# Kernel optimization log

Hardware: AMD Instinct MI355X
Metric: run time of the kernel (lower is better)

Reference implementation:

```python
import jax, jax.numpy as jnp
import numpy as np

CHANNELS = 256
C_QK = CHANNELS // 8


def setup_inputs() -> dict:
    key = jax.random.key(0)
    ks = jax.random.split(key, 7)
    b, c, h, w = 8, CHANNELS, 64, 64
    x = jax.random.normal(ks[0], (b, c, h, w), dtype=jnp.float32)
    # 1x1 conv weights stored as [out_ch, in_ch]; biases [out_ch]
    s = 1.0 / np.sqrt(c)
    wq = jax.random.uniform(ks[1], (C_QK, c), jnp.float32, -s, s)
    bq = jax.random.uniform(ks[2], (C_QK,), jnp.float32, -s, s)
    wk = jax.random.uniform(ks[3], (C_QK, c), jnp.float32, -s, s)
    bk = jax.random.uniform(ks[4], (C_QK,), jnp.float32, -s, s)
    wv = jax.random.uniform(ks[5], (c, c), jnp.float32, -s, s)
    bv = jax.random.uniform(ks[6], (c,), jnp.float32, -s, s)
    return {"x": x, "wq": wq, "bq": bq, "wk": wk, "bk": bk, "wv": wv, "bv": bv}


def reference(x, wq, bq, wk, bk, wv, bv):
    b, c, h, w = x.shape
    xf = x.reshape(b, c, h * w)  # [b, c, n]
    # 1x1 convs == per-pixel linear projections
    q = jnp.einsum('oc,bcn->bon', wq, xf) + bq[None, :, None]  # [b, c//8, n]
    k = jnp.einsum('oc,bcn->bon', wk, xf) + bk[None, :, None]  # [b, c//8, n]
    v = jnp.einsum('oc,bcn->bon', wv, xf) + bv[None, :, None]  # [b, c, n]
    # attention[i, j] = q_i . k_j  (no scaling, matching the torch code)
    attn = jnp.einsum('bdi,bdj->bij', q, k)  # [b, n, n]
    attn = jax.nn.softmax(attn, axis=-1)
    # out[:, :, i] = sum_j attn[i, j] * v[:, :, j]
    out = jnp.einsum('bij,bcj->bci', attn, v)  # [b, c, n]
    return out.reshape(b, c, h, w)
```

## Files before the change

### kernel.cpp

```cpp
#include <hip/hip_runtime.h>
#include <stdint.h>

#define NB 8
#define NC 256
#define ND 32
#define NN 4096
#define QT 64
#define KT 32
#define NBUF 4

typedef __attribute__((ext_vector_type(8))) short short8;
typedef __attribute__((ext_vector_type(4))) float float4_;
typedef __attribute__((ext_vector_type(4))) unsigned int uint4_;

#define MFMA16(a,b,c) __builtin_amdgcn_mfma_f32_16x16x32_bf16((a),(b),(c),0,0,0)

#if __has_builtin(__builtin_amdgcn_exp2f)
#define EXP2(x) __builtin_amdgcn_exp2f(x)
#else
#define EXP2(x) exp2f(x)
#endif
#define L2E 1.44269504088896f
#define SCB (24.0f * L2E)

__device__ __forceinline__ uint16_t f2bf(float f) {
  uint32_t u = __builtin_bit_cast(uint32_t, f);
  u += 0x7fffu + ((u >> 16) & 1u);
  return (uint16_t)(u >> 16);
}
__device__ __forceinline__ float bf2f(uint16_t h) {
  uint32_t u = (uint32_t)h << 16;
  return __builtin_bit_cast(float, u);
}
__device__ __forceinline__ short8 ld8(const uint16_t* p) {
  return *reinterpret_cast<const short8*>(p);
}
__device__ __forceinline__ uint32_t cvtpk(float lo, float hi) {
  uint32_t r;
  asm("v_cvt_pk_bf16_f32 %0, %1, %2" : "=v"(r) : "v"(lo), "v"(hi));
  return r;
}
__device__ __forceinline__ void async16(const uint16_t* g, uint16_t* l) {
  __builtin_amdgcn_global_load_lds(
      (const __attribute__((address_space(1))) uint32_t*)g,
      (__attribute__((address_space(3))) uint32_t*)l, 16, 0, 0);
}
__device__ __forceinline__ void fbar() {
  asm volatile("" ::: "memory");
  __builtin_amdgcn_s_barrier();
  asm volatile("" ::: "memory");
}

__global__ __launch_bounds__(256) void k_prep(
    const float* __restrict__ wq, const float* __restrict__ wk,
    const float* __restrict__ wv,
    uint16_t* __restrict__ WhP, uint16_t* __restrict__ WlP)
{
  int e = blockIdx.x * 256 + threadIdx.x;
  int row = e >> 8, col = e & 255;
  float w = (row < 32) ? wq[e] : (row < 64) ? wk[e - 32 * 256]
                                            : wv[e - 64 * 256];
  uint16_t h = f2bf(w);
  int ks = col >> 5, c5 = col & 31;
  WhP[(size_t)ks * 12800 + row * 40 + c5] = h;
  if (row < 64)
    WlP[(size_t)ks * 2560 + row * 40 + c5] = f2bf(w - bf2f(h));
}

__global__ __launch_bounds__(256) void k_qkv(
    const float* __restrict__ x,
    const uint16_t* __restrict__ WhP, const uint16_t* __restrict__ WlP,
    const float* __restrict__ bq, const float* __restrict__ bk,
    const float* __restrict__ bv,
    uint16_t* __restrict__ Qh, uint16_t* __restrict__ Ql,
    uint16_t* __restrict__ Kh, uint16_t* __restrict__ Kl,
    uint16_t* __restrict__ V, int use_lo)
{
  __shared__ uint32_t xt[64][132];
  __shared__ uint16_t sW[15360];

  int b = blockIdx.x & 7, n0 = (blockIdx.x >> 3) * 64;
  int tid = threadIdx.x, wid = tid >> 6, lane = tid & 63;
  int l15 = lane & 15, quad = lane >> 4;
  int nb = wid * 16;

  auto stageW = [&](int ks) {
    const uint16_t* srcH = WhP + (size_t)ks * 12800;
    const uint16_t* srcL = WlP + (size_t)ks * 2560;
#pragma unroll
    for (int i = 0; i < 8; i++) {
      int idx = i * 256 + tid;
      if (idx < 1920) {
        const uint16_t* g = (idx < 1600) ? (srcH + (size_t)idx * 8)
                                         : (srcL + (size_t)(idx - 1600) * 8);
        async16(g, sW + (size_t)idx * 8);
      }
    }
  };
  auto transpose = [&](int ch) {
    const float* xb = x + ((size_t)b * NC + ch * 128) * NN + n0;
    int cc = tid >> 4, nw = (tid & 15) << 2;
#pragma unroll
    for (int i = 0; i < 8; i++) {
      int c = cc + 16 * i;
      float4_ v = *reinterpret_cast<const float4_*>(xb + (size_t)c * NN + nw);
#pragma unroll
      for (int u = 0; u < 4; u++) {
        uint16_t h = f2bf(v[u]);
        uint16_t l = f2bf(v[u] - bf2f(h));
        xt[nw + u][c] = (uint32_t)h | ((uint32_t)l << 16);
      }
    }
  };

  float4_ acc[20];
  for (int m = 0; m < 20; m++) acc[m] = (float4_){0.f, 0.f, 0.f, 0.f};

  stageW(0);
  transpose(0);
  __syncthreads();

  for (int gks = 0; gks < 8; gks++) {
    int ksl = gks & 3;
    const uint32_t* xr = &xt[nb + l15][ksl * 32 + quad * 8];
    uint4_ r0 = *reinterpret_cast<const uint4_*>(xr);
    uint4_ r1 = *reinterpret_cast<const uint4_*>(xr + 4);
    uint4_ H, L;
    H.x = (r0.x & 0xffffu) | (r0.y << 16);
    L.x = (r0.x >> 16)     | (r0.y & 0xffff0000u);
    H.y = (r0.z & 0xffffu) | (r0.w << 16);
    L.y = (r0.z >> 16)     | (r0.w & 0xffff0000u);
    H.z = (r1.x & 0xffffu) | (r1.y << 16);
    L.z = (r1.x >> 16)     | (r1.y & 0xffff0000u);
    H.w = (r1.z & 0xffffu) | (r1.w << 16);
    L.w = (r1.z >> 16)     | (r1.w & 0xffff0000u);
    short8 bh  = __builtin_bit_cast(short8, H);
    short8 blo = __builtin_bit_cast(short8, L);
#pragma unroll
    for (int mt = 0; mt < 20; mt++) {
      short8 ah = ld8(sW + (16 * mt + l15) * 40 + quad * 8);
      acc[mt] = MFMA16(ah, bh, acc[mt]);
      if (mt < 4) {
        short8 al = ld8(sW + 12800 + (16 * mt + l15) * 40 + quad * 8);
        acc[mt] = MFMA16(al, bh, acc[mt]);
      }
      acc[mt] = MFMA16(ah, blo, acc[mt]);
    }
    __syncthreads();
    if (gks < 7) {
      stageW(gks + 1);
      if (gks == 3) transpose(1);
      __syncthreads();
    }
  }

  int n = n0 + wid * 16 + l15;
  for (int mt = 0; mt < 20; mt++) {
    for (int r = 0; r < 4; r++) {
      int row = 16 * mt + quad * 4 + r;
      float v = acc[mt][r];
      if (mt < 2) {
        v = (v + bq[row]) * L2E;
        size_t o = ((size_t)b * NN + n) * ND + row;
        uint16_t h = f2bf(v);
        Qh[o] = h;
        if (use_lo) Ql[o] = f2bf(v - bf2f(h));
      } else if (mt < 4) {
        int rk = row - 32;
        v += bk[rk];
        size_t o = ((size_t)b * NN + n) * ND + rk;
        uint16_t h = f2bf(v);
        Kh[o] = h;
        if (use_lo) Kl[o] = f2bf(v - bf2f(h));
      } else {
        int c = row - 64;
        v += bv[c];
        V[((size_t)b * NC + c) * NN + n] = f2bf(v);
      }
    }
  }
}

__global__ __launch_bounds__(512, 4) void k_attn(
    const uint16_t* __restrict__ Qh, const uint16_t* __restrict__ Ql,
    const uint16_t* __restrict__ Kh, const uint16_t* __restrict__ Kl,
    const uint16_t* __restrict__ V, float* __restrict__ out, int use_lo)
{
  __shared__ uint16_t sV[NBUF][256][KT];
  __shared__ uint16_t sP[2][4][16][40];
  __shared__ float sL[QT];

  int bx = blockIdx.x;
  int b = bx & 7;
  int q0 = (bx >> 3) * QT;
  int tid = threadIdx.x, wid = tid >> 6, lane = tid & 63;
  int l15 = lane & 15, quad = lane >> 4;
  const size_t qkb = (size_t)b * NN * ND;
  const uint16_t* Vb = V + (size_t)b * NC * NN;
  const bool heavy = (wid < 4);

  int sw = (l15 >> 1) & 3;

  const uint16_t* gp0; const uint16_t* gp1;
  const uint16_t* gp2; const uint16_t* gp3;
  uint32_t off0, off1, off2, off3;
  if (!heavy) {
#define INITGP(i, GP, OFF)                                   \
    { int sl = (wid - 4) * 256 + 64 * i + lane;              \
      int c = sl >> 2;                                       \
      int q2s = (sl & 3) ^ ((sl >> 3) & 3);                  \
      GP = Vb + (size_t)c * NN + q2s * 8;                    \
      OFF = (uint32_t)(((wid - 4) * 4 + i) * 512); }
    INITGP(0, gp0, off0) INITGP(1, gp1, off1)
    INITGP(2, gp2, off2) INITGP(3, gp3, off3)
#undef INITGP
  }
  auto stage = [&](int s) {
    uint16_t* base = &sV[0][0][0] + (size_t)(s & 3) * 8192;
    async16(gp0, base + off0); gp0 += KT;
    async16(gp1, base + off1); gp1 += KT;
    async16(gp2, base + off2); gp2 += KT;
    async16(gp3, base + off3); gp3 += KT;
  };

  float4_ acc[2][4];
  for (int m = 0; m < 2; m++) for (int n = 0; n < 4; n++)
    acc[m][n] = (float4_){0.f, 0.f, 0.f, 0.f};
  float l_part = 0.f;

  short8 qfh, qfl, kh0, kh1, kl0, kl1;
  const uint16_t* pKh = Kh + qkb + (size_t)l15 * ND + quad * 8;
  const uint16_t* pKl = Kl + qkb + (size_t)l15 * ND + quad * 8;

  auto qkt = [&](int sb, short8 h0, short8 h1, short8 lo0, short8 lo1) {
    float4_ S0 = (float4_){0.f, 0.f, 0.f, 0.f}, S1 = S0;
    S0 = MFMA16(h0, qfh, S0);
    S1 = MFMA16(h1, qfh, S1);
    if (use_lo) {
      S0 = MFMA16(lo0, qfh, S0); S0 = MFMA16(h0, qfl, S0);
      S1 = MFMA16(lo1, qfh, S1); S1 = MFMA16(h1, qfl, S1);
    }
    float p0[4], p1[4];
#pragma unroll
    for (int r = 0; r < 4; r++) {
      p0[r] = EXP2(S0[r] - SCB);
      p1[r] = EXP2(S1[r] - SCB);
    }
    l_part += ((p0[0] + p0[1]) + (p0[2] + p0[3])) +
              ((p1[0] + p1[1]) + (p1[2] + p1[3]));
    uint2 w0, w1;
    w0.x = cvtpk(p0[0], p0[1]); w0.y = cvtpk(p0[2], p0[3]);
    w1.x = cvtpk(p1[0], p1[1]); w1.y = cvtpk(p1[2], p1[3]);
    *reinterpret_cast<uint2*>(&sP[sb][wid][l15][4 * quad]) = w0;
    *reinterpret_cast<uint2*>(&sP[sb][wid][l15][16 + 4 * quad]) = w1;
  };

  if (heavy) {
    size_t a = qkb + (size_t)(q0 + wid * 16 + l15) * ND + quad * 8;
    qfh = ld8(Qh + a);
    if (use_lo) qfl = ld8(Ql + a);
    short8 t0 = ld8(pKh), t1 = ld8(pKh + 512), tl0, tl1;
    if (use_lo) { tl0 = ld8(pKl); tl1 = ld8(pKl + 512); }
    qkt(0, t0, t1, tl0, tl1);
    kh0 = ld8(pKh + 1024); kh1 = ld8(pKh + 1536);
    if (use_lo) { kl0 = ld8(pKl + 1024); kl1 = ld8(pKl + 1536); }
    pKh += 2048; pKl += 2048;
    asm volatile("s_waitcnt lgkmcnt(0)" ::: "memory");
  } else {
    stage(0); stage(1); stage(2);
    asm volatile("s_waitcnt vmcnt(8)" ::: "memory");
  }
  fbar();

  for (int j = 0; j < NN / KT; j++) {
    int buf = j & 3;
    int pb = j & 1;
    if (heavy) {
      short8 nh0, nh1, nl0, nl1;
      if (j < NN / KT - 2) {
        nh0 = ld8(pKh); nh1 = ld8(pKh + 512);
        if (use_lo) { nl0 = ld8(pKl); nl1 = ld8(pKl + 512); }
        pKh += 1024; pKl += 1024;
      }
      if (j < NN / KT - 1)
        qkt(pb ^ 1, kh0, kh1, kl0, kl1);
      kh0 = nh0; kh1 = nh1;
      if (use_lo) { kl0 = nl0; kl1 = nl1; }
    } else {
      if (j < NN / KT - 3) stage(j + 3);
    }
    short8 bfP[4];
#pragma unroll
    for (int qt = 0; qt < 4; qt++)
      bfP[qt] = ld8(&sP[pb][qt][l15][quad * 8]);
#pragma unroll
    for (int mt = 0; mt < 2; mt++) {
      short8 af = ld8(&sV[buf][wid * 32 + 16 * mt + l15][(quad ^ sw) * 8]);
#pragma unroll
      for (int qt = 0; qt < 4; qt++)
        acc[mt][qt] = MFMA16(af, bfP[qt], acc[mt][qt]);
    }
    if (!heavy) {
      if (j < NN / KT - 3)
        asm volatile("s_waitcnt vmcnt(8)" ::: "memory");
      else
        asm volatile("s_waitcnt vmcnt(0)" ::: "memory");
    }
    asm volatile("s_waitcnt lgkmcnt(0)" ::: "memory");
    fbar();
  }

  if (heavy) {
    float l_tot = l_part;
    l_tot += __shfl_xor(l_tot, 16);
    l_tot += __shfl_xor(l_tot, 32);
    if (quad == 0) sL[wid * 16 + l15] = l_tot;
  }
  __syncthreads();
  float linv[4];
  for (int qt = 0; qt < 4; qt++) linv[qt] = 1.0f / sL[qt * 16 + l15];
  for (int mt = 0; mt < 2; mt++)
    for (int qt = 0; qt < 4; qt++)
      for (int r = 0; r < 4; r++) {
        int c = wid * 32 + 16 * mt + quad * 4 + r;
        int q = q0 + qt * 16 + l15;
        out[((size_t)(b * NC + c)) * NN + q] = acc[mt][qt][r] * linv[qt];
      }
}

extern "C" void kernel_launch(void* const* d_in, const int* in_sizes, int n_in,
                              void* d_out, int out_size, void* d_ws, size_t ws_size,
                              hipStream_t stream)
{
  const float* x  = (const float*)d_in[0];
  const float* wq = (const float*)d_in[1];
  const float* bq = (const float*)d_in[2];
  const float* wk = (const float*)d_in[3];
  const float* bk = (const float*)d_in[4];
  const float* wv = (const float*)d_in[5];
  const float* bv = (const float*)d_in[6];
  float* out = (float*)d_out;

  const size_t szWh = (size_t)8 * 320 * 40 * 2;
  const size_t szWl = (size_t)8 * 64 * 40 * 2;
  const size_t szQK = (size_t)NB * NN * ND * 2;
  const size_t szV  = (size_t)NB * NC * NN * 2;
  size_t needB = szWh + szWl + 4 * szQK + szV;
  int use_lo = ws_size >= needB;

  char* p = (char*)d_ws;
  uint16_t* WhP = (uint16_t*)p; p += szWh;
  uint16_t* WlP = (uint16_t*)p; p += szWl;
  uint16_t* Qh = (uint16_t*)p; p += szQK;
  uint16_t* Ql = use_lo ? (uint16_t*)p : Qh; if (use_lo) p += szQK;
  uint16_t* Kh = (uint16_t*)p; p += szQK;
  uint16_t* Kl = use_lo ? (uint16_t*)p : Kh; if (use_lo) p += szQK;
  uint16_t* Vw = (uint16_t*)p;

  hipLaunchKernelGGL(k_prep, dim3(320), dim3(256), 0, stream,
                     wq, wk, wv, WhP, WlP);
  hipLaunchKernelGGL(k_qkv, dim3(512), dim3(256), 0, stream,
                     x, WhP, WlP, bq, bk, bv, Qh, Ql, Kh, Kl, Vw, use_lo);
  hipLaunchKernelGGL(k_attn, dim3(512), dim3(512), 0, stream,
                     Qh, Ql, Kh, Kl, Vw, out, use_lo);
}
```

Before: 235.7 us.

## Double key tile to 64 and repartition QK^T work across heavy waves by key

```diff
diff --git a/kernel.cpp b/kernel.cpp
--- a/kernel.cpp
+++ b/kernel.cpp
@@ -6,7 +6,7 @@
 #define ND 32
 #define NN 4096
 #define QT 64
-#define KT 32
+#define KT 64
 #define NBUF 4
 
 typedef __attribute__((ext_vector_type(8))) short short8;
@@ -181,14 +181,14 @@
   }
 }
 
-__global__ __launch_bounds__(512, 4) void k_attn(
+__global__ __launch_bounds__(512, 2) void k_attn(
     const uint16_t* __restrict__ Qh, const uint16_t* __restrict__ Ql,
     const uint16_t* __restrict__ Kh, const uint16_t* __restrict__ Kl,
     const uint16_t* __restrict__ V, float* __restrict__ out, int use_lo)
 {
   __shared__ uint16_t sV[NBUF][256][KT];
-  __shared__ uint16_t sP[2][4][16][40];
-  __shared__ float sL[QT];
+  __shared__ uint16_t sP[2][4][16][72];
+  __shared__ float sL[4][QT];
 
   int bx = blockIdx.x;
   int b = bx & 7;
@@ -199,109 +199,113 @@
   const uint16_t* Vb = V + (size_t)b * NC * NN;
   const bool heavy = (wid < 4);
 
-  int sw = (l15 >> 1) & 3;
-
-  const uint16_t* gp0; const uint16_t* gp1;
-  const uint16_t* gp2; const uint16_t* gp3;
-  uint32_t off0, off1, off2, off3;
+  const uint16_t* gp[8];
+  uint32_t off[8];
   if (!heavy) {
-#define INITGP(i, GP, OFF)                                   \
-    { int sl = (wid - 4) * 256 + 64 * i + lane;              \
-      int c = sl >> 2;                                       \
-      int q2s = (sl & 3) ^ ((sl >> 3) & 3);                  \
-      GP = Vb + (size_t)c * NN + q2s * 8;                    \
-      OFF = (uint32_t)(((wid - 4) * 4 + i) * 512); }
-    INITGP(0, gp0, off0) INITGP(1, gp1, off1)
-    INITGP(2, gp2, off2) INITGP(3, gp3, off3)
-#undef INITGP
+#pragma unroll
+    for (int i = 0; i < 8; i++) {
+      int sl = (wid - 4) * 512 + i * 64 + lane;
+      int c = sl >> 3;
+      int k8s = (sl & 7) ^ (c & 7);
+      gp[i] = Vb + (size_t)c * NN + k8s * 8;
+      off[i] = (uint32_t)sl * 8;
+    }
   }
   auto stage = [&](int s) {
-    uint16_t* base = &sV[0][0][0] + (size_t)(s & 3) * 8192;
-    async16(gp0, base + off0); gp0 += KT;
-    async16(gp1, base + off1); gp1 += KT;
-    async16(gp2, base + off2); gp2 += KT;
-    async16(gp3, base + off3); gp3 += KT;
+    uint16_t* base = &sV[0][0][0] + (size_t)(s & 3) * 16384;
+#pragma unroll
+    for (int i = 0; i < 8; i++) {
+      async16(gp[i], base + off[i]);
+      gp[i] += KT;
+    }
   };
 
   float4_ acc[2][4];
   for (int m = 0; m < 2; m++) for (int n = 0; n < 4; n++)
     acc[m][n] = (float4_){0.f, 0.f, 0.f, 0.f};
-  float l_part = 0.f;
-
-  short8 qfh, qfl, kh0, kh1, kl0, kl1;
-  const uint16_t* pKh = Kh + qkb + (size_t)l15 * ND + quad * 8;
-  const uint16_t* pKl = Kl + qkb + (size_t)l15 * ND + quad * 8;
-
-  auto qkt = [&](int sb, short8 h0, short8 h1, short8 lo0, short8 lo1) {
-    float4_ S0 = (float4_){0.f, 0.f, 0.f, 0.f}, S1 = S0;
-    S0 = MFMA16(h0, qfh, S0);
-    S1 = MFMA16(h1, qfh, S1);
-    if (use_lo) {
-      S0 = MFMA16(lo0, qfh, S0); S0 = MFMA16(h0, qfl, S0);
-      S1 = MFMA16(lo1, qfh, S1); S1 = MFMA16(h1, qfl, S1);
-    }
-    float p0[4], p1[4];
-#pragma unroll
-    for (int r = 0; r < 4; r++) {
-      p0[r] = EXP2(S0[r] - SCB);
-      p1[r] = EXP2(S1[r] - SCB);
-    }
-    l_part += ((p0[0] + p0[1]) + (p0[2] + p0[3])) +
-              ((p1[0] + p1[1]) + (p1[2] + p1[3]));
-    uint2 w0, w1;
-    w0.x = cvtpk(p0[0], p0[1]); w0.y = cvtpk(p0[2], p0[3]);
-    w1.x = cvtpk(p1[0], p1[1]); w1.y = cvtpk(p1[2], p1[3]);
-    *reinterpret_cast<uint2*>(&sP[sb][wid][l15][4 * quad]) = w0;
-    *reinterpret_cast<uint2*>(&sP[sb][wid][l15][16 + 4 * quad]) = w1;
+  float lp[4] = {0.f, 0.f, 0.f, 0.f};
+
+  short8 qfh[4], qfl[4], kh, klv;
+  const uint16_t* pKh = Kh + qkb + (size_t)(wid * 16 + l15) * ND + quad * 8;
+  const uint16_t* pKl = Kl + qkb + (size_t)(wid * 16 + l15) * ND + quad * 8;
+
+  auto qkt4 = [&](int sb, short8 h, short8 lo) {
+#pragma unroll
+    for (int qg = 0; qg < 4; qg++) {
+      float4_ S = (float4_){0.f, 0.f, 0.f, 0.f};
+      S = MFMA16(h, qfh[qg], S);
+      if (use_lo) {
+        S = MFMA16(lo, qfh[qg], S);
+        S = MFMA16(h, qfl[qg], S);
+      }
+      float p[4];
+#pragma unroll
+      for (int r = 0; r < 4; r++) p[r] = EXP2(S[r] - SCB);
+      lp[qg] += (p[0] + p[1]) + (p[2] + p[3]);
+      uint2 w;
+      w.x = cvtpk(p[0], p[1]);
+      w.y = cvtpk(p[2], p[3]);
+      *reinterpret_cast<uint2*>(&sP[sb][qg][l15][wid * 16 + 4 * quad]) = w;
+    }
   };
 
   if (heavy) {
-    size_t a = qkb + (size_t)(q0 + wid * 16 + l15) * ND + quad * 8;
-    qfh = ld8(Qh + a);
-    if (use_lo) qfl = ld8(Ql + a);
-    short8 t0 = ld8(pKh), t1 = ld8(pKh + 512), tl0, tl1;
-    if (use_lo) { tl0 = ld8(pKl); tl1 = ld8(pKl + 512); }
-    qkt(0, t0, t1, tl0, tl1);
-    kh0 = ld8(pKh + 1024); kh1 = ld8(pKh + 1536);
-    if (use_lo) { kl0 = ld8(pKl + 1024); kl1 = ld8(pKl + 1536); }
-    pKh += 2048; pKl += 2048;
+#pragma unroll
+    for (int qg = 0; qg < 4; qg++) {
+      size_t qa = qkb + (size_t)(q0 + qg * 16 + l15) * ND + quad * 8;
+      qfh[qg] = ld8(Qh + qa);
+      if (use_lo) qfl[qg] = ld8(Ql + qa);
+    }
+    short8 t0 = ld8(pKh), tl0;
+    if (use_lo) tl0 = ld8(pKl);
+    qkt4(0, t0, tl0);
+    kh = ld8(pKh + 2048);
+    if (use_lo) klv = ld8(pKl + 2048);
+    pKh += 4096; pKl += 4096;
     asm volatile("s_waitcnt lgkmcnt(0)" ::: "memory");
   } else {
-    stage(0); stage(1); stage(2);
+    stage(0); stage(1);
     asm volatile("s_waitcnt vmcnt(8)" ::: "memory");
   }
   fbar();
 
-  for (int j = 0; j < NN / KT; j++) {
+  const int NIT = NN / KT;
+  for (int j = 0; j < NIT; j++) {
     int buf = j & 3;
     int pb = j & 1;
     if (heavy) {
-      short8 nh0, nh1, nl0, nl1;
-      if (j < NN / KT - 2) {
-        nh0 = ld8(pKh); nh1 = ld8(pKh + 512);
-        if (use_lo) { nl0 = ld8(pKl); nl1 = ld8(pKl + 512); }
-        pKh += 1024; pKl += 1024;
-      }
-      if (j < NN / KT - 1)
-        qkt(pb ^ 1, kh0, kh1, kl0, kl1);
-      kh0 = nh0; kh1 = nh1;
-      if (use_lo) { kl0 = nl0; kl1 = nl1; }
+      short8 nh, nl;
+      if (j < NIT - 2) {
+        nh = ld8(pKh);
+        if (use_lo) nl = ld8(pKl);
+        pKh += 2048; pKl += 2048;
+      }
+      if (j < NIT - 1)
+        qkt4(pb ^ 1, kh, klv);
+      kh = nh;
+      if (use_lo) klv = nl;
     } else {
-      if (j < NN / KT - 3) stage(j + 3);
-    }
-    short8 bfP[4];
-#pragma unroll
-    for (int qt = 0; qt < 4; qt++)
-      bfP[qt] = ld8(&sP[pb][qt][l15][quad * 8]);
+      if (j < NIT - 2) stage(j + 2);
+    }
+    short8 bfP[4][2];
+#pragma unroll
+    for (int qg = 0; qg < 4; qg++)
+#pragma unroll
+      for (int kh2 = 0; kh2 < 2; kh2++)
+        bfP[qg][kh2] = ld8(&sP[pb][qg][l15][kh2 * 32 + quad * 8]);
 #pragma unroll
     for (int mt = 0; mt < 2; mt++) {
-      short8 af = ld8(&sV[buf][wid * 32 + 16 * mt + l15][(quad ^ sw) * 8]);
-#pragma unroll
-      for (int qt = 0; qt < 4; qt++)
-        acc[mt][qt] = MFMA16(af, bfP[qt], acc[mt][qt]);
+      int row = wid * 32 + 16 * mt + l15;
+#pragma unroll
+      for (int kh2 = 0; kh2 < 2; kh2++) {
+        short8 af = ld8(&sV[buf][row][(((kh2 << 2) + quad) ^ (l15 & 7)) << 3]);
+#pragma unroll
+        for (int qg = 0; qg < 4; qg++)
+          acc[mt][qg] = MFMA16(af, bfP[qg][kh2], acc[mt][qg]);
+      }
     }
     if (!heavy) {
-      if (j < NN / KT - 3)
+      if (j < NIT - 2)
         asm volatile("s_waitcnt vmcnt(8)" ::: "memory");
       else
         asm volatile("s_waitcnt vmcnt(0)" ::: "memory");
@@ -311,16 +315,25 @@
   }
 
   if (heavy) {
-    float l_tot = l_part;
-    l_tot += __shfl_xor(l_tot, 16);
-    l_tot += __shfl_xor(l_tot, 32);
-    if (quad == 0) sL[wid * 16 + l15] = l_tot;
+#pragma unroll
+    for (int qg = 0; qg < 4; qg++) {
+      float t = lp[qg];
+      t += __shfl_xor(t, 16);
+      t += __shfl_xor(t, 32);
+      if (quad == 0) sL[wid][qg * 16 + l15] = t;
+    }
   }
   __syncthreads();
   float linv[4];
-  for (int qt = 0; qt < 4; qt++) linv[qt] = 1.0f / sL[qt * 16 + l15];
+#pragma unroll
+  for (int qt = 0; qt < 4; qt++)
+    linv[qt] = 1.0f / (sL[0][qt * 16 + l15] + sL[1][qt * 16 + l15] +
+                       sL[2][qt * 16 + l15] + sL[3][qt * 16 + l15]);
+#pragma unroll
   for (int mt = 0; mt < 2; mt++)
+#pragma unroll
     for (int qt = 0; qt < 4; qt++)
+#pragma unroll
       for (int r = 0; r < 4; r++) {
         int c = wid * 32 + 16 * mt + quad * 4 + r;
         int q = q0 + qt * 16 + l15;
```

New measurement: 262.8 us. +11.5%, slower.

## Double-buffer QKV projection stages and swizzle transposed x tile in LDS

Applied to the files above, without the earlier changes.

```diff
diff --git a/kernel.cpp b/kernel.cpp
--- a/kernel.cpp
+++ b/kernel.cpp
@@ -76,53 +76,62 @@
     uint16_t* __restrict__ Kh, uint16_t* __restrict__ Kl,
     uint16_t* __restrict__ V, int use_lo)
 {
-  __shared__ uint32_t xt[64][132];
-  __shared__ uint16_t sW[15360];
+  __shared__ uint32_t xt2[2][64][36];
+  __shared__ uint16_t sW[2][15360];
 
   int b = blockIdx.x & 7, n0 = (blockIdx.x >> 3) * 64;
   int tid = threadIdx.x, wid = tid >> 6, lane = tid & 63;
   int l15 = lane & 15, quad = lane >> 4;
-  int nb = wid * 16;
-
-  auto stageW = [&](int ks) {
+
+  auto stageW = [&](int ks, int bf) {
     const uint16_t* srcH = WhP + (size_t)ks * 12800;
     const uint16_t* srcL = WlP + (size_t)ks * 2560;
+    uint16_t* dst = &sW[bf][0];
 #pragma unroll
     for (int i = 0; i < 8; i++) {
       int idx = i * 256 + tid;
       if (idx < 1920) {
         const uint16_t* g = (idx < 1600) ? (srcH + (size_t)idx * 8)
                                          : (srcL + (size_t)(idx - 1600) * 8);
-        async16(g, sW + (size_t)idx * 8);
+        async16(g, dst + (size_t)idx * 8);
       }
     }
   };
-  auto transpose = [&](int ch) {
-    const float* xb = x + ((size_t)b * NC + ch * 128) * NN + n0;
-    int cc = tid >> 4, nw = (tid & 15) << 2;
-#pragma unroll
-    for (int i = 0; i < 8; i++) {
-      int c = cc + 16 * i;
-      float4_ v = *reinterpret_cast<const float4_*>(xb + (size_t)c * NN + nw);
-#pragma unroll
-      for (int u = 0; u < 4; u++) {
-        uint16_t h = f2bf(v[u]);
-        uint16_t l = f2bf(v[u] - bf2f(h));
-        xt[nw + u][c] = (uint32_t)h | ((uint32_t)l << 16);
-      }
+  auto transposeS = [&](int g, int bf) {
+    int c = tid >> 3;
+    int nq = (tid & 7) << 3;
+    const float* xb = x + ((size_t)b * NC + 32 * g + c) * NN + n0 + nq;
+    float4_ v0 = *reinterpret_cast<const float4_*>(xb);
+    float4_ v1 = *reinterpret_cast<const float4_*>(xb + 4);
+#pragma unroll
+    for (int u = 0; u < 8; u++) {
+      float v = (u < 4) ? v0[u] : v1[u - 4];
+      uint16_t h = f2bf(v);
+      uint16_t l = f2bf(v - bf2f(h));
+      int n = nq + u;
+      int cs = c ^ (((n >> 3) & 3) << 3);
+      xt2[bf][n][cs] = (uint32_t)h | ((uint32_t)l << 16);
     }
   };
 
   float4_ acc[20];
   for (int m = 0; m < 20; m++) acc[m] = (float4_){0.f, 0.f, 0.f, 0.f};
 
-  stageW(0);
-  transpose(0);
-  __syncthreads();
-
-  for (int gks = 0; gks < 8; gks++) {
-    int ksl = gks & 3;
-    const uint32_t* xr = &xt[nb + l15][ksl * 32 + quad * 8];
+  stageW(0, 0);
+  transposeS(0, 0);
+  asm volatile("s_waitcnt vmcnt(0) lgkmcnt(0)" ::: "memory");
+  fbar();
+
+  int n_ = wid * 16 + l15;
+  int swz = ((n_ >> 3) & 3) << 3;
+
+  for (int g = 0; g < 8; g++) {
+    int bf = g & 1;
+    if (g < 7) {
+      stageW(g + 1, bf ^ 1);
+      transposeS(g + 1, bf ^ 1);
+    }
+    const uint32_t* xr = &xt2[bf][n_][(quad << 3) ^ swz];
     uint4_ r0 = *reinterpret_cast<const uint4_*>(xr);
     uint4_ r1 = *reinterpret_cast<const uint4_*>(xr + 4);
     uint4_ H, L;
@@ -136,22 +145,19 @@
     L.w = (r1.z >> 16)     | (r1.w & 0xffff0000u);
     short8 bh  = __builtin_bit_cast(short8, H);
     short8 blo = __builtin_bit_cast(short8, L);
+    const uint16_t* wb = &sW[bf][0];
 #pragma unroll
     for (int mt = 0; mt < 20; mt++) {
-      short8 ah = ld8(sW + (16 * mt + l15) * 40 + quad * 8);
+      short8 ah = ld8(wb + (16 * mt + l15) * 40 + quad * 8);
       acc[mt] = MFMA16(ah, bh, acc[mt]);
       if (mt < 4) {
-        short8 al = ld8(sW + 12800 + (16 * mt + l15) * 40 + quad * 8);
+        short8 al = ld8(wb + 12800 + (16 * mt + l15) * 40 + quad * 8);
         acc[mt] = MFMA16(al, bh, acc[mt]);
       }
       acc[mt] = MFMA16(ah, blo, acc[mt]);
     }
-    __syncthreads();
-    if (gks < 7) {
-      stageW(gks + 1);
-      if (gks == 3) transpose(1);
-      __syncthreads();
-    }
+    asm volatile("s_waitcnt vmcnt(0) lgkmcnt(0)" ::: "memory");
+    fbar();
   }
 
   int n = n0 + wid * 16 + l15;
```

New measurement: 234.3 us, median of 2. Within noise of the previous version (-0.6%).
